# Optimization experiments

Hardware: AMD Instinct MI355X
Metric: run time of the kernel (lower is better)

## Reference

```python
import jax, jax.numpy as jnp
import numpy as np

THR = 1.0      # spiking threshold for encoder and hidden LIF neurons
ALPHA = 0.9    # hidden membrane leak
BETA = 0.9     # output (leaky-integrator) membrane leak
SUR_K = 10.0   # surrogate-gradient sharpness (fwd unaffected)


def _spike(v):
    # Hard Heaviside in fwd, sigmoid surrogate in bwd (straight-through)
    sur = jax.nn.sigmoid(SUR_K * (v - THR))
    hard = (v >= THR).astype(v.dtype)
    return sur + jax.lax.stop_gradient(hard - sur)


def setup_inputs() -> dict:
    key = jax.random.key(0)
    k1, k2, k3 = jax.random.split(key, 3)
    B, T, ORDER, H, C = 512, 1024, 128, 1024, 10
    x = jax.random.normal(k1, (B, T, ORDER), dtype=jnp.float32)
    W_hdn = jax.random.normal(k2, (2 * ORDER, H), dtype=jnp.float32) * (1.0 / np.sqrt(2 * ORDER))
    W_otp = jax.random.normal(k3, (H, C), dtype=jnp.float32) * (1.0 / np.sqrt(H))
    return {"x": x, "W_hdn": W_hdn, "W_otp": W_otp}


def reference(x, W_hdn, W_otp):
    # x: (B, T, ORDER). States are reset (zeros) at the start of each forward,
    # mirroring reset_v()/reset_states() in the torch module.
    B, T, ORDER = x.shape
    H = W_hdn.shape[1]
    C = W_otp.shape[1]
    dt = x.dtype

    xt = jnp.transpose(x, (1, 0, 2))  # (T, B, ORDER) for scan

    def step(carry, x_t):
        v_e, v_h, v_o = carry
        # EncoderLayer: on/off rectified channels -> IF neuron with soft reset
        cur = jnp.concatenate([jax.nn.relu(x_t), jax.nn.relu(-x_t)], axis=-1)  # (B, 2*ORDER)
        v_e = v_e + cur
        s_e = _spike(v_e)
        v_e = v_e - s_e * THR
        # HiddenLayer: LIF with leak ALPHA, soft reset
        v_h = ALPHA * v_h + s_e @ W_hdn
        s_h = _spike(v_h)
        v_h = v_h - s_h * THR
        # OutputLayer: non-spiking leaky integrator; emit membrane potential
        v_o = BETA * v_o + s_h @ W_otp
        return (v_e, v_h, v_o), v_o

    init = (
        jnp.zeros((B, 2 * ORDER), dtype=dt),
        jnp.zeros((B, H), dtype=dt),
        jnp.zeros((B, C), dtype=dt),
    )
    _, m_pots = jax.lax.scan(step, init, xt)  # (T, B, C)
    return jnp.transpose(m_pots, (1, 0, 2))   # (B, T, C) == all_m_pots
```

## Files before the change

kernel.cpp:

```cpp
#include <hip/hip_runtime.h>
#include <hip/hip_bf16.h>


#define BB 512
#define TT 1024
#define OO 128
#define KK 256
#define HH 1024
#define CC 10
#define TC 64
#define NCHUNK (TT / TC)

typedef unsigned long long u64;
typedef __attribute__((ext_vector_type(8))) short short8;
typedef __attribute__((ext_vector_type(4))) float floatx4;
typedef __attribute__((ext_vector_type(4))) int intx4;

__device__ __forceinline__ unsigned short f2bf_rn(float f) {
    unsigned u = __float_as_uint(f);
    u += 0x7FFFu + ((u >> 16) & 1u);
    return (unsigned short)(u >> 16);
}
__device__ __forceinline__ float bf2f(unsigned short h) {
    return __uint_as_float(((unsigned)h) << 16);
}

__global__ __launch_bounds__(128) void k_enc(const float* __restrict__ x,
                                             u64* __restrict__ me) {
    const int b    = blockIdx.x;
    const int j    = threadIdx.x;
    const int wv   = j >> 6;
    const int lane = j & 63;
    const float* xb = x + (size_t)b * (TT * OO);
    float vp = 0.f, vn = 0.f;
    for (int t0 = 0; t0 < TT; t0 += 16) {
        float xs[16];
#pragma unroll
        for (int g = 0; g < 16; ++g) xs[g] = xb[(t0 + g) * OO + j];
#pragma unroll
        for (int g = 0; g < 16; ++g) {
            float xv = xs[g];
            float cp = fmaxf(xv, 0.f);
            float cn = fmaxf(-xv, 0.f);
            vp += cp;
            vn += cn;
            bool sp = (vp >= 1.0f);
            bool sn = (vn >= 1.0f);
            u64 mp = __ballot(sp);
            u64 mn = __ballot(sn);
            if (sp) vp -= 1.0f;
            if (sn) vn -= 1.0f;
            if (lane == 0) {
                size_t r = ((size_t)b * TT + (t0 + g)) * 4;
                me[r + wv]     = mp;
                me[r + 2 + wv] = mn;
            }
        }
    }
}

__global__ __launch_bounds__(256) void k_quant(const float* __restrict__ Wh,
                                               unsigned short* __restrict__ Wt) {
    int idx = blockIdx.x * 256 + threadIdx.x;
    int n = idx >> 9;
    int k = idx & 511;
    float w = Wh[(size_t)(k & 255) * HH + n];
    unsigned short hi = f2bf_rn(w);
    unsigned short out = (k < KK) ? hi : f2bf_rn(w - bf2f(hi));
    Wt[(size_t)n * 512 + k] = out;
}

__global__ __launch_bounds__(256) void k_quant_o(const float* __restrict__ Wo,
                                                 unsigned short* __restrict__ Wqo) {
    int idx = blockIdx.x * 256 + threadIdx.x;
    int n = idx >> 11;
    int k = idx & 2047;
    unsigned short out = 0;
    if (n < CC) {
        float w = Wo[(size_t)(k & 1023) * CC + n];
        unsigned short hi = f2bf_rn(w);
        out = (k < HH) ? hi : f2bf_rn(w - bf2f(hi));
    }
    Wqo[(size_t)n * 2048 + k] = out;
}

__global__ __launch_bounds__(256, 2) void k_gemm_scan(
    const u64* __restrict__ me, const unsigned short* __restrict__ Wt,
    float* __restrict__ vstate, u64* __restrict__ mh, int t0) {
    __shared__ __align__(16) char smem[66560];
    char* Blds = smem;
    char* Lut  = smem + 16384;
    u64*  Mlds = (u64*)(smem + 20480);
    float* Scr = (float*)smem;

    const int tid  = threadIdx.x;
    const int wave = tid >> 6;
    const int lane = tid & 63;
    const int quad = lane >> 4;
    const int l15  = lane & 15;
    const int mtile = blockIdx.x;
    const int ny    = blockIdx.y;

    {
        int m  = mtile * 256 + tid;
        int b  = m >> 6;
        int tl = m & 63;
        size_t base = ((size_t)b * TT + (t0 + tl)) * 4;
        Mlds[tid * 4 + 0] = me[base + 0];
        Mlds[tid * 4 + 1] = me[base + 1];
        Mlds[tid * 4 + 2] = me[base + 2];
        Mlds[tid * 4 + 3] = me[base + 3];
        unsigned e = (unsigned)tid;
        unsigned p0 = ((e >> 0) & 1) * 0x3F80u | ((e >> 1) & 1) * 0x3F800000u;
        unsigned p1 = ((e >> 2) & 1) * 0x3F80u | ((e >> 3) & 1) * 0x3F800000u;
        unsigned p2 = ((e >> 4) & 1) * 0x3F80u | ((e >> 5) & 1) * 0x3F800000u;
        unsigned p3 = ((e >> 6) & 1) * 0x3F80u | ((e >> 7) & 1) * 0x3F800000u;
        ((intx4*)Lut)[tid] = intx4{(int)p0, (int)p1, (int)p2, (int)p3};
    }

    floatx4 acc[4][8];
#pragma unroll
    for (int i = 0; i < 4; ++i)
#pragma unroll
        for (int j2 = 0; j2 < 8; ++j2) acc[i][j2] = floatx4{0.f, 0.f, 0.f, 0.f};

    for (int kt = 0; kt < 8; ++kt) {
        __syncthreads();
        {
            int nl = tid >> 1;
            int cpart = tid & 1;
            const intx4* src = (const intx4*)(Wt + ((size_t)(ny * 128 + nl) * 512 + kt * 64));
#pragma unroll
            for (int p2 = 0; p2 < 4; ++p2) {
                int jj = cpart * 4 + p2;
                intx4 val = src[jj];
                *((intx4*)(Blds + nl * 128 + ((jj ^ (nl & 7)) * 16))) = val;
            }
        }
        __syncthreads();
        u64 aw[4];
#pragma unroll
        for (int mg = 0; mg < 4; ++mg) {
            int row = wave * 64 + mg * 16 + l15;
            aw[mg] = Mlds[row * 4 + (kt & 3)];
        }
#pragma unroll
        for (int kw = 0; kw < 2; ++kw) {
            int shift = kw * 32 + quad * 8;
            short8 afrag[4];
#pragma unroll
            for (int mg = 0; mg < 4; ++mg) {
                unsigned byte = (unsigned)((aw[mg] >> shift) & 0xFFu);
                afrag[mg] = *((const short8*)(Lut + byte * 16));
            }
#pragma unroll
            for (int ng = 0; ng < 8; ++ng) {
                int brow = ng * 16 + l15;
                int jj = kw * 4 + quad;
                short8 bfrag = *((const short8*)(Blds + brow * 128 + ((jj ^ (brow & 7)) * 16)));
#pragma unroll
                for (int mg = 0; mg < 4; ++mg)
                    acc[mg][ng] = __builtin_amdgcn_mfma_f32_16x16x32_bf16(
                        afrag[mg], bfrag, acc[mg][ng], 0, 0, 0);
            }
        }
    }

    const int b = mtile * 4 + wave;
    float* scr = Scr + wave * (64 * 65);
#pragma unroll
    for (int h = 0; h < 2; ++h) {
        __syncthreads();
#pragma unroll
        for (int mg = 0; mg < 4; ++mg)
#pragma unroll
            for (int ng2 = 0; ng2 < 4; ++ng2) {
                int ng = h * 4 + ng2;
#pragma unroll
                for (int r = 0; r < 4; ++r) {
                    int rowt = mg * 16 + quad * 4 + r;
                    int col  = ng2 * 16 + l15;
                    scr[rowt * 65 + col] = acc[mg][ng][r];
                }
            }
        __syncthreads();
        int ngl = ny * 128 + h * 64 + lane;
        float v = vstate[(size_t)b * HH + ngl];
        for (int tl = 0; tl < TC; ++tl) {
            float c = scr[tl * 65 + lane];
            v = 0.9f * v + c;
            bool s = (v >= 1.0f);
            u64 wm = __ballot(s);
            if (s) v -= 1.0f;
            if (lane == 0) mh[((size_t)b * TT + (t0 + tl)) * 16 + ny * 2 + h] = wm;
        }
        vstate[(size_t)b * HH + ngl] = v;
    }
}

__global__ __launch_bounds__(256, 2) void k_outcur_mfma(
    const u64* __restrict__ mh, const unsigned short* __restrict__ Wqo,
    float* __restrict__ I) {
    __shared__ __align__(16) char smem[69632];
    char* Bo  = smem;
    char* Lut = smem + 65536;

    const int tid  = threadIdx.x;
    const int wave = tid >> 6;
    const int lane = tid & 63;
    const int quad = lane >> 4;
    const int l15  = lane & 15;

    {
#pragma unroll
        for (int i = 0; i < 16; ++i) {
            int pid = i * 256 + tid;
            int n = pid >> 8, p = pid & 255;
            intx4 v = ((const intx4*)Wqo)[pid];
            *((intx4*)(Bo + n * 4096 + ((p ^ (n & 7)) * 16))) = v;
        }
        unsigned e = (unsigned)tid;
        unsigned p0 = ((e >> 0) & 1) * 0x3F80u | ((e >> 1) & 1) * 0x3F800000u;
        unsigned p1 = ((e >> 2) & 1) * 0x3F80u | ((e >> 3) & 1) * 0x3F800000u;
        unsigned p2 = ((e >> 4) & 1) * 0x3F80u | ((e >> 5) & 1) * 0x3F800000u;
        unsigned p3 = ((e >> 6) & 1) * 0x3F80u | ((e >> 7) & 1) * 0x3F800000u;
        ((intx4*)(Lut))[tid] = intx4{(int)p0, (int)p1, (int)p2, (int)p3};
    }
    __syncthreads();

    const int tbase = blockIdx.x * 16 + wave * 4;
    floatx4 acc[4];
#pragma unroll
    for (int tt = 0; tt < 4; ++tt) acc[tt] = floatx4{0.f, 0.f, 0.f, 0.f};

    const u64* rowp[4];
#pragma unroll
    for (int tt = 0; tt < 4; ++tt)
        rowp[tt] = mh + ((size_t)(tbase + tt) * 16 + l15) * 16;

    for (int wi = 0; wi < 16; ++wi) {
        u64 w[4];
#pragma unroll
        for (int tt = 0; tt < 4; ++tt) w[tt] = rowp[tt][wi];
#pragma unroll
        for (int half = 0; half < 2; ++half) {
            int shift = half * 32 + quad * 8;
            int kt_hi = 2 * wi + half;
            int kt_lo = 32 + kt_hi;
            int j_hi = kt_hi * 4 + quad;
            int j_lo = kt_lo * 4 + quad;
            short8 bhi = *((const short8*)(Bo + l15 * 4096 + ((j_hi ^ (l15 & 7)) * 16)));
            short8 blo = *((const short8*)(Bo + l15 * 4096 + ((j_lo ^ (l15 & 7)) * 16)));
#pragma unroll
            for (int tt = 0; tt < 4; ++tt) {
                unsigned byte = (unsigned)((w[tt] >> shift) & 0xFFu);
                short8 af = *((const short8*)(Lut + byte * 16));
                acc[tt] = __builtin_amdgcn_mfma_f32_16x16x32_bf16(af, bhi, acc[tt], 0, 0, 0);
                acc[tt] = __builtin_amdgcn_mfma_f32_16x16x32_bf16(af, blo, acc[tt], 0, 0, 0);
            }
        }
    }

#pragma unroll
    for (int tt = 0; tt < 4; ++tt)
#pragma unroll
        for (int r = 0; r < 4; ++r) {
            int m = (tbase + tt) * 16 + quad * 4 + r;
            if (l15 < CC) I[(size_t)m * CC + l15] = acc[tt][r];
        }
}

__global__ __launch_bounds__(192) void k_integ1(const float* __restrict__ I,
                                                float* __restrict__ out,
                                                float* __restrict__ vend) {
    int b = blockIdx.x;
    int tid = threadIdx.x;
    if (tid >= 160) return;
    int chunk = tid / 10, c = tid % 10;
    int t0 = chunk * 64;
    const float* Ib = I + ((size_t)b * TT + t0) * CC + c;
    float* ob = out + ((size_t)b * TT + t0) * CC + c;
    float v = 0.f;
    for (int g0 = 0; g0 < 64; g0 += 8) {
        float xs[8];
#pragma unroll
        for (int g = 0; g < 8; ++g) xs[g] = Ib[(g0 + g) * CC];
#pragma unroll
        for (int g = 0; g < 8; ++g) {
            v = 0.9f * v + xs[g];
            ob[(g0 + g) * CC] = v;
        }
    }
    vend[((size_t)b * 16 + chunk) * CC + c] = v;
}

__global__ __launch_bounds__(256) void k_integ2(const float* __restrict__ vend,
                                                float* __restrict__ carry) {
    int id = blockIdx.x * 256 + threadIdx.x;
    if (id >= BB * CC) return;
    int b = id / CC, c = id % CC;
    float d64 = 1.f;
#pragma unroll
    for (int i = 0; i < 64; ++i) d64 *= 0.9f;
    float cv = 0.f;
    for (int k = 0; k < 16; ++k) {
        carry[((size_t)b * 16 + k) * CC + c] = cv;
        cv = vend[((size_t)b * 16 + k) * CC + c] + d64 * cv;
    }
}

__global__ __launch_bounds__(256) void k_integ3(const float* __restrict__ carry,
                                                float* __restrict__ out) {
    __shared__ float dec[64];
    if (threadIdx.x == 0) {
        float d = 1.f;
        for (int i = 0; i < 64; ++i) { d *= 0.9f; dec[i] = d; }
    }
    __syncthreads();
    size_t id = (size_t)blockIdx.x * 256 + threadIdx.x;
    int c = (int)(id % CC);
    size_t bt = id / CC;
    int t = (int)(bt % TT);
    int b = (int)(bt / TT);
    int chunk = t >> 6, tl = t & 63;
    out[id] += dec[tl] * carry[((size_t)b * 16 + chunk) * CC + c];
}

extern "C" void kernel_launch(void* const* d_in, const int* in_sizes, int n_in,
                              void* d_out, int out_size, void* d_ws, size_t ws_size,
                              hipStream_t stream) {
    const float* x  = (const float*)d_in[0];
    const float* Wh = (const float*)d_in[1];
    const float* Wo = (const float*)d_in[2];

    char* p = (char*)d_ws;
    u64* me = (u64*)p;                        p += (size_t)BB * TT * 4 * 8;
    u64* mh = (u64*)p;                        p += (size_t)BB * TT * 16 * 8;
    unsigned short* Wt = (unsigned short*)p;  p += (size_t)HH * 512 * 2;
    float* vstate = (float*)p;                p += (size_t)BB * HH * 4;
    float* I = (float*)p;                     p += (size_t)BB * TT * CC * 4;
    unsigned short* Wqo = (unsigned short*)p; p += (size_t)16 * 2048 * 2;
    float* vend  = (float*)Wt;
    float* carry = (float*)(Wt + 512 * 512);

    hipMemsetAsync(vstate, 0, (size_t)BB * HH * 4, stream);
    hipLaunchKernelGGL(k_enc, dim3(BB), dim3(128), 0, stream, x, me);
    hipLaunchKernelGGL(k_quant, dim3(2048), dim3(256), 0, stream, Wh, Wt);
    hipLaunchKernelGGL(k_quant_o, dim3(128), dim3(256), 0, stream, Wo, Wqo);
    for (int ct = 0; ct < NCHUNK; ++ct)
        hipLaunchKernelGGL(k_gemm_scan, dim3(128, 8), dim3(256), 0, stream,
                           me, Wt, vstate, mh, ct * TC);
    hipLaunchKernelGGL(k_outcur_mfma, dim3(2048), dim3(256), 0, stream, mh, Wqo, I);
    hipLaunchKernelGGL(k_integ1, dim3(BB), dim3(192), 0, stream, I, (float*)d_out, vend);
    hipLaunchKernelGGL(k_integ2, dim3(20), dim3(256), 0, stream, vend, carry);
    hipLaunchKernelGGL(k_integ3, dim3(20480), dim3(256), 0, stream, carry, (float*)d_out);
}
```

Before: 1.264 ms.

## Fuse time-chunk loop into one persistent gemm-scan kernel with register-held state

```diff
diff --git a/kernel.cpp b/kernel.cpp
--- a/kernel.cpp
+++ b/kernel.cpp
@@ -60,14 +60,16 @@
 }
 
 __global__ __launch_bounds__(256) void k_quant(const float* __restrict__ Wh,
-                                               unsigned short* __restrict__ Wt) {
+                                               unsigned short* __restrict__ Wt2) {
     int idx = blockIdx.x * 256 + threadIdx.x;
     int n = idx >> 9;
     int k = idx & 511;
     float w = Wh[(size_t)(k & 255) * HH + n];
     unsigned short hi = f2bf_rn(w);
     unsigned short out = (k < KK) ? hi : f2bf_rn(w - bf2f(hi));
-    Wt[(size_t)n * 512 + k] = out;
+    int kt = k >> 6, kw = (k >> 5) & 1, q = (k >> 3) & 3, e = k & 7;
+    size_t C = (size_t)(kt * 2 + kw) * 4096 + n * 4 + q;
+    Wt2[C * 8 + e] = out;
 }
 
 __global__ __launch_bounds__(256) void k_quant_o(const float* __restrict__ Wo,
@@ -85,13 +87,11 @@
 }
 
 __global__ __launch_bounds__(256, 2) void k_gemm_scan(
-    const u64* __restrict__ me, const unsigned short* __restrict__ Wt,
-    float* __restrict__ vstate, u64* __restrict__ mh, int t0) {
-    __shared__ __align__(16) char smem[66560];
-    char* Blds = smem;
-    char* Lut  = smem + 16384;
-    u64*  Mlds = (u64*)(smem + 20480);
-    float* Scr = (float*)smem;
+    const u64* __restrict__ me, const unsigned short* __restrict__ Wt2,
+    u64* __restrict__ mh) {
+    __shared__ __align__(16) char smem[4096 + 4 * 8192];
+    char*  Lut    = smem;
+    float* ScrAll = (float*)(smem + 4096);
 
     const int tid  = threadIdx.x;
     const int wave = tid >> 6;
@@ -100,16 +100,10 @@
     const int l15  = lane & 15;
     const int mtile = blockIdx.x;
     const int ny    = blockIdx.y;
+    const int b     = mtile * 4 + wave;
+    float* scr = ScrAll + wave * 2048;
 
     {
-        int m  = mtile * 256 + tid;
-        int b  = m >> 6;
-        int tl = m & 63;
-        size_t base = ((size_t)b * TT + (t0 + tl)) * 4;
-        Mlds[tid * 4 + 0] = me[base + 0];
-        Mlds[tid * 4 + 1] = me[base + 1];
-        Mlds[tid * 4 + 2] = me[base + 2];
-        Mlds[tid * 4 + 3] = me[base + 3];
         unsigned e = (unsigned)tid;
         unsigned p0 = ((e >> 0) & 1) * 0x3F80u | ((e >> 1) & 1) * 0x3F800000u;
         unsigned p1 = ((e >> 2) & 1) * 0x3F80u | ((e >> 3) & 1) * 0x3F800000u;
@@ -117,84 +111,80 @@
         unsigned p3 = ((e >> 6) & 1) * 0x3F80u | ((e >> 7) & 1) * 0x3F800000u;
         ((intx4*)Lut)[tid] = intx4{(int)p0, (int)p1, (int)p2, (int)p3};
     }
-
-    floatx4 acc[4][8];
-#pragma unroll
-    for (int i = 0; i < 4; ++i)
-#pragma unroll
-        for (int j2 = 0; j2 < 8; ++j2) acc[i][j2] = floatx4{0.f, 0.f, 0.f, 0.f};
-
-    for (int kt = 0; kt < 8; ++kt) {
-        __syncthreads();
-        {
-            int nl = tid >> 1;
-            int cpart = tid & 1;
-            const intx4* src = (const intx4*)(Wt + ((size_t)(ny * 128 + nl) * 512 + kt * 64));
-#pragma unroll
-            for (int p2 = 0; p2 < 4; ++p2) {
-                int jj = cpart * 4 + p2;
-                intx4 val = src[jj];
-                *((intx4*)(Blds + nl * 128 + ((jj ^ (nl & 7)) * 16))) = val;
-            }
-        }
-        __syncthreads();
-        u64 aw[4];
-#pragma unroll
-        for (int mg = 0; mg < 4; ++mg) {
-            int row = wave * 64 + mg * 16 + l15;
-            aw[mg] = Mlds[row * 4 + (kt & 3)];
-        }
-#pragma unroll
-        for (int kw = 0; kw < 2; ++kw) {
-            int shift = kw * 32 + quad * 8;
-            short8 afrag[4];
-#pragma unroll
-            for (int mg = 0; mg < 4; ++mg) {
-                unsigned byte = (unsigned)((aw[mg] >> shift) & 0xFFu);
-                afrag[mg] = *((const short8*)(Lut + byte * 16));
-            }
-#pragma unroll
-            for (int ng = 0; ng < 8; ++ng) {
-                int brow = ng * 16 + l15;
-                int jj = kw * 4 + quad;
-                short8 bfrag = *((const short8*)(Blds + brow * 128 + ((jj ^ (brow & 7)) * 16)));
-#pragma unroll
-                for (int mg = 0; mg < 4; ++mg)
-                    acc[mg][ng] = __builtin_amdgcn_mfma_f32_16x16x32_bf16(
-                        afrag[mg], bfrag, acc[mg][ng], 0, 0, 0);
-            }
-        }
-    }
-
-    const int b = mtile * 4 + wave;
-    float* scr = Scr + wave * (64 * 65);
-#pragma unroll
-    for (int h = 0; h < 2; ++h) {
-        __syncthreads();
-#pragma unroll
-        for (int mg = 0; mg < 4; ++mg)
-#pragma unroll
-            for (int ng2 = 0; ng2 < 4; ++ng2) {
-                int ng = h * 4 + ng2;
-#pragma unroll
-                for (int r = 0; r < 4; ++r) {
-                    int rowt = mg * 16 + quad * 4 + r;
-                    int col  = ng2 * 16 + l15;
-                    scr[rowt * 65 + col] = acc[mg][ng][r];
+    __syncthreads();
+
+    const short8* Bp = (const short8*)Wt2;
+    const int swz = (l15 + (l15 >> 2)) & 3;
+    float va = 0.f, vb = 0.f;
+
+#pragma unroll 1
+    for (int ct = 0; ct < NCHUNK; ++ct) {
+        const int t0 = ct * TC;
+
+        floatx4 acc[4][8];
+#pragma unroll
+        for (int i = 0; i < 4; ++i)
+#pragma unroll
+            for (int j2 = 0; j2 < 8; ++j2) acc[i][j2] = floatx4{0.f, 0.f, 0.f, 0.f};
+
+#pragma unroll 1
+        for (int kt = 0; kt < 8; ++kt) {
+            u64 aw[4];
+#pragma unroll
+            for (int mg = 0; mg < 4; ++mg)
+                aw[mg] = me[((size_t)b * TT + (t0 + mg * 16 + l15)) * 4 + (kt & 3)];
+#pragma unroll
+            for (int kw = 0; kw < 2; ++kw) {
+                const int shift = kw * 32 + quad * 8;
+                short8 afrag[4];
+#pragma unroll
+                for (int mg = 0; mg < 4; ++mg) {
+                    unsigned byte = (unsigned)((aw[mg] >> shift) & 0xFFu);
+                    afrag[mg] = *((const short8*)(Lut + byte * 16));
+                }
+                const size_t cbase = (size_t)(kt * 2 + kw) * 4096 + ny * 512
+                                   + l15 * 4 + quad;
+#pragma unroll
+                for (int ng = 0; ng < 8; ++ng) {
+                    short8 bfrag = Bp[cbase + ng * 64];
+#pragma unroll
+                    for (int mg = 0; mg < 4; ++mg)
+                        acc[mg][ng] = __builtin_amdgcn_mfma_f32_16x16x32_bf16(
+                            afrag[mg], bfrag, acc[mg][ng], 0, 0, 0);
                 }
             }
-        __syncthreads();
-        int ngl = ny * 128 + h * 64 + lane;
-        float v = vstate[(size_t)b * HH + ngl];
-        for (int tl = 0; tl < TC; ++tl) {
-            float c = scr[tl * 65 + lane];
-            v = 0.9f * v + c;
-            bool s = (v >= 1.0f);
-            u64 wm = __ballot(s);
-            if (s) v -= 1.0f;
-            if (lane == 0) mh[((size_t)b * TT + (t0 + tl)) * 16 + ny * 2 + h] = wm;
-        }
-        vstate[(size_t)b * HH + ngl] = v;
+        }
+
+#pragma unroll 1
+        for (int mg = 0; mg < 4; ++mg) {
+#pragma unroll
+            for (int ng = 0; ng < 8; ++ng)
+                *((floatx4*)(scr + (ng * 16 + l15) * 16 + ((quad ^ swz) << 2))) =
+                    acc[mg][ng];
+#pragma unroll
+            for (int tt = 0; tt < 4; ++tt) {
+                const int rsw = ((tt ^ swz) << 2);
+                floatx4 ca = *((const floatx4*)(scr + lane * 16 + rsw));
+                floatx4 cb = *((const floatx4*)(scr + (lane + 64) * 16 + rsw));
+#pragma unroll
+                for (int r = 0; r < 4; ++r) {
+                    const int t = t0 + mg * 16 + tt * 4 + r;
+                    va = fmaf(0.9f, va, ca[r]);
+                    vb = fmaf(0.9f, vb, cb[r]);
+                    bool sa = (va >= 1.0f);
+                    bool sb = (vb >= 1.0f);
+                    u64 ma = __ballot(sa);
+                    u64 mb = __ballot(sb);
+                    if (sa) va -= 1.0f;
+                    if (sb) vb -= 1.0f;
+                    if (lane == 0) {
+                        u64* mp = mh + ((size_t)b * TT + t) * 16 + ny * 2;
+                        mp[0] = ma;
+                        mp[1] = mb;
+                    }
+                }
+            }
+        }
     }
 }
 
@@ -337,19 +327,15 @@
     u64* me = (u64*)p;                        p += (size_t)BB * TT * 4 * 8;
     u64* mh = (u64*)p;                        p += (size_t)BB * TT * 16 * 8;
     unsigned short* Wt = (unsigned short*)p;  p += (size_t)HH * 512 * 2;
-    float* vstate = (float*)p;                p += (size_t)BB * HH * 4;
     float* I = (float*)p;                     p += (size_t)BB * TT * CC * 4;
     unsigned short* Wqo = (unsigned short*)p; p += (size_t)16 * 2048 * 2;
     float* vend  = (float*)Wt;
     float* carry = (float*)(Wt + 512 * 512);
 
-    hipMemsetAsync(vstate, 0, (size_t)BB * HH * 4, stream);
     hipLaunchKernelGGL(k_enc, dim3(BB), dim3(128), 0, stream, x, me);
     hipLaunchKernelGGL(k_quant, dim3(2048), dim3(256), 0, stream, Wh, Wt);
     hipLaunchKernelGGL(k_quant_o, dim3(128), dim3(256), 0, stream, Wo, Wqo);
-    for (int ct = 0; ct < NCHUNK; ++ct)
-        hipLaunchKernelGGL(k_gemm_scan, dim3(128, 8), dim3(256), 0, stream,
-                           me, Wt, vstate, mh, ct * TC);
+    hipLaunchKernelGGL(k_gemm_scan, dim3(128, 8), dim3(256), 0, stream, me, Wt, mh);
     hipLaunchKernelGGL(k_outcur_mfma, dim3(2048), dim3(256), 0, stream, mh, Wqo, I);
     hipLaunchKernelGGL(k_integ1, dim3(BB), dim3(192), 0, stream, I, (float*)d_out, vend);
     hipLaunchKernelGGL(k_integ2, dim3(20), dim3(256), 0, stream, vend, carry);
```

Result: slower. 1.646 ms (+30.2%).
